# Performance work log

Hardware: AMD Instinct MI355X
Metric: run time of the kernel (lower is better)

The kernel has to match this reference:

```python
import jax, jax.numpy as jnp
import numpy as np

P, N, F, H, D_HID = 3, 4096, 1024, 8, 8
EMBED = H * D_HID  # 64
ATT, C = 128, 16


def setup_inputs() -> dict:
    key = jax.random.key(0)
    ks = jax.random.split(key, 12)
    return {
        "inputs": jax.random.normal(ks[0], (P, N, F), jnp.float32),
        # bias_mat plays the role of an additive adjacency mask; random floats are fine for math checking
        "bias_mat": jax.random.normal(ks[1], (P, N, N), jnp.float32),
        "W": jax.random.normal(ks[2], (P, H, F, D_HID), jnp.float32) * 0.05,
        "a1_w": jax.random.normal(ks[3], (P, H, D_HID), jnp.float32) * 0.1,
        "a1_b": jax.random.normal(ks[4], (P, H), jnp.float32) * 0.1,
        "a2_w": jax.random.normal(ks[5], (P, H, D_HID), jnp.float32) * 0.1,
        "a2_b": jax.random.normal(ks[6], (P, H), jnp.float32) * 0.1,
        "h_bias": jnp.zeros((P, H, D_HID), jnp.float32),
        "Ws": jax.random.normal(ks[7], (EMBED, ATT), jnp.float32) * 0.1,
        "bs": jax.random.normal(ks[8], (ATT,), jnp.float32) * 0.1,
        "u": jax.random.normal(ks[9], (ATT,), jnp.float32) * 0.1,
        "Wc": jax.random.normal(ks[10], (EMBED, C), jnp.float32) * 0.05,
        "bc": jnp.zeros((C,), jnp.float32),
    }


def reference(inputs, bias_mat, W, a1_w, a1_b, a2_w, a2_b, h_bias, Ws, bs, u, Wc, bc):
    # inputs: [P,N,F], bias_mat: [P,N,N]
    embeds = []
    for p in range(inputs.shape[0]):  # small fixed loop over meta-paths
        seq = inputs[p]                                            # [N,F]
        fts = jnp.einsum('nf,hfd->hnd', seq, W[p])                 # shared projection, all heads
        f1 = jnp.einsum('hnd,hd->hn', fts, a1_w[p]) + a1_b[p][:, None]
        f2 = jnp.einsum('hnd,hd->hn', fts, a2_w[p]) + a2_b[p][:, None]
        logits = f1[:, :, None] + f2[:, None, :]                   # [H,N,N] additive attention
        coefs = jax.nn.softmax(jax.nn.leaky_relu(logits) + bias_mat[p][None], axis=-1)
        vals = jnp.einsum('hnm,hmd->hnd', coefs, fts) + h_bias[p][:, None, :]
        h = jax.nn.elu(vals)                                       # activation per head
        embeds.append(jnp.transpose(h, (1, 0, 2)).reshape(h.shape[1], -1))  # concat heads -> [N,H*d]
    multi = jnp.stack(embeds, axis=1)                              # [N,P,EMBED]
    # semantic (meta-path) attention
    v = jnp.tanh(multi @ Ws + bs)                                  # [N,P,ATT]
    alphas = jax.nn.softmax(v @ u, axis=-1)                        # [N,P]
    final = jnp.sum(multi * alphas[:, :, None], axis=1)            # [N,EMBED]
    # single final classifier head (mean over 1 head == identity)
    logits_out = final @ Wc + bc                                   # [N,C]
    return logits_out, final, alphas
```

## Files before the change

kernel.cpp:

```cpp
#include <hip/hip_runtime.h>

#define LOG2E 1.44269504088896f

typedef _Float16 f16;
typedef _Float16 f16x8 __attribute__((ext_vector_type(8)));
typedef float f32x4 __attribute__((ext_vector_type(4)));

#define NP 3
#define NN 4096
#define FF 1024
#define HH 8
#define DD 8
#define HD 64

#define OFF_F1S   0
#define OFF_F2S   393216
#define OFF_F2MAX 589824
#define OFF_FTST  590080
#define OFF_MULTI 2162944

#define OUT_FINAL 65536
#define OUT_ALPHA 327680

__global__ __launch_bounds__(256) void kA(const float* __restrict__ inp,
                                          const float* __restrict__ W,
                                          const float* __restrict__ a1w,
                                          const float* __restrict__ a1b,
                                          const float* __restrict__ a2w,
                                          const float* __restrict__ a2b,
                                          char* __restrict__ ws) {
    __shared__ float At[32 * 34];
    __shared__ float Bt[32 * 64];
    __shared__ float ftile[32 * 68];
    const int tid = threadIdx.x;
    const int p = blockIdx.y;
    const int n0 = blockIdx.x * 32;

    const int tr = tid >> 4, tc = tid & 15;
    const int r0 = tr * 2, c0 = tc * 4;
    const int sr = tid >> 3, sak = (tid & 7) * 4;
    const int bk = tid >> 3, bh = tid & 7;

    const float* aP = inp + ((size_t)p * NN + n0 + sr) * FF + sak;
    const float* bP = W + (((size_t)p * HH + bh) * FF + bk) * DD;
    float* bDst = &Bt[bk * 64 + bh * 8];

    float4 pa, pb0, pb1;

#define KA_ISSUE(kb) do { \
        pa = *(const float4*)(aP + (kb) * 32); \
        const float* bp_ = bP + (size_t)(kb) * 32 * DD; \
        pb0 = *(const float4*)(bp_); \
        pb1 = *(const float4*)(bp_ + 4); \
    } while (0)

#define KA_COMMIT() do { \
        At[(sak + 0) * 34 + sr] = pa.x; \
        At[(sak + 1) * 34 + sr] = pa.y; \
        At[(sak + 2) * 34 + sr] = pa.z; \
        At[(sak + 3) * 34 + sr] = pa.w; \
        *(float4*)(bDst) = pb0; \
        *(float4*)(bDst + 4) = pb1; \
    } while (0)

    float acc[2][4] = {};

    KA_ISSUE(0);
    KA_COMMIT();
    KA_ISSUE(1);
    __syncthreads();

    #pragma unroll 1
    for (int kb = 0; kb < 32; ++kb) {
        #pragma unroll
        for (int k = 0; k < 32; ++k) {
            float2 a2 = *(const float2*)&At[k * 34 + r0];
            float4 bv = *(const float4*)&Bt[k * 64 + c0];
            float bb4[4] = {bv.x, bv.y, bv.z, bv.w};
            #pragma unroll
            for (int j = 0; j < 4; ++j) {
                acc[0][j] += a2.x * bb4[j];
                acc[1][j] += a2.y * bb4[j];
            }
        }
        __syncthreads();
        if (kb < 31) {
            KA_COMMIT();
            if (kb < 30) KA_ISSUE(kb + 2);
            __syncthreads();
        }
    }
#undef KA_ISSUE
#undef KA_COMMIT

    #pragma unroll
    for (int i = 0; i < 2; ++i) {
        float4 o;
        o.x = acc[i][0]; o.y = acc[i][1]; o.z = acc[i][2]; o.w = acc[i][3];
        *(float4*)&ftile[(r0 + i) * 68 + c0] = o;
    }
    __syncthreads();

    float* f1s = (float*)(ws + OFF_F1S);
    f16* f2s = (f16*)(ws + OFF_F2S);
    {
        int row = tid >> 3, h = tid & 7;
        const float* fb = &ftile[row * 68 + h * 8];
        float s1 = a1b[p * HH + h], s2 = a2b[p * HH + h];
        #pragma unroll
        for (int d = 0; d < 8; ++d) {
            float v = fb[d];
            s1 += v * a1w[((size_t)p * HH + h) * DD + d];
            s2 += v * a2w[((size_t)p * HH + h) * DD + d];
        }
        f1s[((size_t)p * HH + h) * NN + n0 + row] = s1 * LOG2E;
        f2s[((size_t)p * HH + h) * NN + n0 + row] = (f16)(s2 * LOG2E);
    }
    {
        f16* ftsT = (f16*)(ws + OFF_FTST);
        int cc2 = tid >> 2, rq = (tid & 3) * 8;
        union { f16 h[8]; uint4 u; } pk;
        #pragma unroll
        for (int i = 0; i < 8; ++i) pk.h[i] = (f16)ftile[(rq + i) * 68 + cc2];
        *(uint4*)(ftsT + ((size_t)p * HD + cc2) * NN + n0 + rq) = pk.u;
    }
}

__global__ __launch_bounds__(64) void kA2(char* __restrict__ ws) {
    const f16* f2s = (const f16*)(ws + OFF_F2S);
    float* fmax = (float*)(ws + OFF_F2MAX);
    int b = blockIdx.x;
    int lane = threadIdx.x;
    float v = -1e30f;
    for (int m = lane; m < NN; m += 64) v = fmaxf(v, (float)f2s[(size_t)b * NN + m]);
    #pragma unroll
    for (int off = 32; off >= 1; off >>= 1) v = fmaxf(v, __shfl_xor(v, off, 64));
    if (lane == 0) fmax[b] = v;
}

__global__ __launch_bounds__(256, 3) void kB(const float* __restrict__ bias,
                                             const float* __restrict__ h_bias,
                                             char* __restrict__ ws) {
    __shared__ __align__(16) char smem[42768];
    f16* ftsL = (f16*)smem;
    float* f2L = (float*)(smem + 34320);

    const int tid = threadIdx.x;
    const int lane = tid & 63, wv = tid >> 6;
    const int c = lane & 15, kg = lane >> 4;
    const int p = blockIdx.y;
    const int n0 = blockIdx.x * 16;
    const int n = n0 + c;

    const float* f1s = (const float*)(ws + OFF_F1S);
    const f16* f2s = (const f16*)(ws + OFF_F2S);
    const float* fmax = (const float*)(ws + OFF_F2MAX);
    const f16* ftsG = (const f16*)(ws + OFF_FTST);
    float* multi = (float*)(ws + OFF_MULTI);

    float A1[8], B1[8];
    #pragma unroll
    for (int h = 0; h < 8; ++h) {
        float f1v = f1s[((size_t)p * 8 + h) * NN + n];
        float fm = fmax[p * 8 + h];
        float x = f1v + fm;
        float lr = fmaxf(x, 0.01f * x);
        float ub = lr + 8.0f * LOG2E;
        A1[h] = f1v - ub;
        B1[h] = fmaf(0.01f, f1v, -ub);
    }

    for (int i = tid; i < 264; i += 256) ftsL[64 * 264 + i] = (f16)1.0f;

    const int sg = tid >> 3, se = tid & 7;
    const int srow = sg & 7, sq = sg >> 3;
    const int f2r = tid >> 5, f2c = (tid & 31) * 8;

    const f16* ftsP = ftsG + (size_t)p * HD * NN + sq * 64 + se * 8;
    const f16* f2P = f2s + (size_t)p * 8 * NN + (size_t)f2r * NN + f2c;
    f16* ldst = ftsL + srow * 264 + sq * 64 + se * 8;

    const int rowsel = (c < 8) ? c * 264 : 64 * 264;
    const int hstep = (c < 8) ? 8 * 264 : 0;

    const float* bb_base = bias + ((size_t)p * NN + n) * NN + wv * 64 + kg * 8;

    f32x4 acc[8] = {};

    uint4 r0, r1, r2, r3, r4, r5, r6, r7, rv;

#define ISSUE(ch) do { \
        const f16* gs_ = ftsP + (ch) * 256; \
        r0 = *(const uint4*)(gs_ + (size_t)(srow +  0) * NN); \
        r1 = *(const uint4*)(gs_ + (size_t)(srow +  8) * NN); \
        r2 = *(const uint4*)(gs_ + (size_t)(srow + 16) * NN); \
        r3 = *(const uint4*)(gs_ + (size_t)(srow + 24) * NN); \
        r4 = *(const uint4*)(gs_ + (size_t)(srow + 32) * NN); \
        r5 = *(const uint4*)(gs_ + (size_t)(srow + 40) * NN); \
        r6 = *(const uint4*)(gs_ + (size_t)(srow + 48) * NN); \
        r7 = *(const uint4*)(gs_ + (size_t)(srow + 56) * NN); \
        rv = *(const uint4*)(f2P + (ch) * 256); \
    } while (0)

#define COMMIT() do { \
        *(uint4*)(ldst + 0 * 8 * 264) = r0; \
        *(uint4*)(ldst + 1 * 8 * 264) = r1; \
        *(uint4*)(ldst + 2 * 8 * 264) = r2; \
        *(uint4*)(ldst + 3 * 8 * 264) = r3; \
        *(uint4*)(ldst + 4 * 8 * 264) = r4; \
        *(uint4*)(ldst + 5 * 8 * 264) = r5; \
        *(uint4*)(ldst + 6 * 8 * 264) = r6; \
        *(uint4*)(ldst + 7 * 8 * 264) = r7; \
        union { uint4 u; f16 h[8]; } t16_; \
        t16_.u = rv; \
        float4 lo_, hi_; \
        lo_.x = (float)t16_.h[0]; lo_.y = (float)t16_.h[1]; \
        lo_.z = (float)t16_.h[2]; lo_.w = (float)t16_.h[3]; \
        hi_.x = (float)t16_.h[4]; hi_.y = (float)t16_.h[5]; \
        hi_.z = (float)t16_.h[6]; hi_.w = (float)t16_.h[7]; \
        *(float4*)(f2L + f2r * 264 + f2c) = lo_; \
        *(float4*)(f2L + f2r * 264 + f2c + 4) = hi_; \
    } while (0)

    ISSUE(0);
    COMMIT();
    ISSUE(1);
    float4 uA0 = *(const float4*)(bb_base);
    float4 uA1 = *(const float4*)(bb_base + 4);
    float4 uB0 = *(const float4*)(bb_base + 32);
    float4 uB1 = *(const float4*)(bb_base + 36);
    __syncthreads();

    #pragma unroll 1
    for (int ch = 0; ch < 16; ++ch) {
        const int chn = (ch + 1 < 16) ? ch + 1 : 15;
        const float* bpn = bb_base + chn * 256;
        float4 nA0 = *(const float4*)(bpn);
        float4 nA1 = *(const float4*)(bpn + 4);
        float4 nB0 = *(const float4*)(bpn + 32);
        float4 nB1 = *(const float4*)(bpn + 36);

        #pragma unroll
        for (int s = 0; s < 2; ++s) {
            const int mloc = wv * 64 + s * 32 + kg * 8;
            float4 bv0 = s ? uB0 : uA0;
            float4 bv1 = s ? uB1 : uA1;
            float bbl[8] = {bv0.x * LOG2E, bv0.y * LOG2E, bv0.z * LOG2E, bv0.w * LOG2E,
                            bv1.x * LOG2E, bv1.y * LOG2E, bv1.z * LOG2E, bv1.w * LOG2E};
            #pragma unroll
            for (int h = 0; h < 8; ++h) {
                const float* f2p = f2L + h * 264 + mloc;
                float4 f2a = *(const float4*)f2p;
                float4 f2b = *(const float4*)(f2p + 4);
                float f2arr[8] = {f2a.x, f2a.y, f2a.z, f2a.w, f2b.x, f2b.y, f2b.z, f2b.w};
                f16x8 bf = *(const f16x8*)(ftsL + rowsel + h * hstep + mloc);
                union { f16x8 v; f16 e[8]; } af;
                #pragma unroll
                for (int j = 0; j < 8; ++j) {
                    float t1 = f2arr[j] + A1[h];
                    float t2 = fmaf(0.01f, f2arr[j], B1[h]);
                    af.e[j] = (f16)__builtin_amdgcn_exp2f(fmaxf(t1, t2) + bbl[j]);
                }
                acc[h] = __builtin_amdgcn_mfma_f32_16x16x32_f16(af.v, bf, acc[h], 0, 0, 0);
            }
        }
        __syncthreads();
        if (ch < 15) {
            COMMIT();
            if (ch < 14) ISSUE(ch + 2);
            __syncthreads();
        }
        uA0 = nA0; uA1 = nA1; uB0 = nB0; uB1 = nB1;
    }
#undef ISSUE
#undef COMMIT

    float* red = (float*)smem;
    #pragma unroll
    for (int h = 0; h < 8; ++h) {
        if (c <= 8) {
            #pragma unroll
            for (int r = 0; r < 4; ++r)
                red[((wv * 8 + h) * 16 + kg * 4 + r) * 9 + c] = acc[h][r];
        }
    }
    __syncthreads();
    #pragma unroll
    for (int rep = 0; rep < 4; ++rep) {
        int idx = tid + rep * 256;
        int R = idx >> 6, hd = idx & 63;
        int h = hd >> 3, d = hd & 7;
        float v = 0.f, l = 0.f;
        #pragma unroll
        for (int w = 0; w < 4; ++w) {
            v += red[((w * 8 + h) * 16 + R) * 9 + d];
            l += red[((w * 8 + h) * 16 + R) * 9 + 8];
        }
        float o = v / l + h_bias[(p * 8 + h) * 8 + d];
        o = o > 0.f ? o : (__builtin_amdgcn_exp2f(o * LOG2E) - 1.0f);
        multi[((size_t)(n0 + R) * NP + p) * HD + hd] = o;
    }
}

__global__ __launch_bounds__(256) void kC(const float* __restrict__ Ws,
                                          const float* __restrict__ bsv,
                                          const float* __restrict__ uv,
                                          const float* __restrict__ Wc,
                                          const float* __restrict__ bcv,
                                          char* __restrict__ ws,
                                          float* __restrict__ out) {
    __shared__ float WsL[64 * 128];
    __shared__ float mult[16 * 3 * 64];
    __shared__ float WcL[64 * 16];
    __shared__ float uL[128], bsL[128], bcL[16];
    __shared__ float vred[16 * 3 * 16];
    __shared__ float alphaL[16 * 3];
    __shared__ float fin[16 * 64];
    const int tid = threadIdx.x;
    const int n0 = blockIdx.x * 16;
    const float* multi = (const float*)(ws + OFF_MULTI);

    for (int i = tid; i < 64 * 128; i += 256) WsL[i] = Ws[i];
    for (int i = tid; i < 3072; i += 256) mult[i] = multi[(size_t)n0 * 192 + i];
    for (int i = tid; i < 1024; i += 256) WcL[i] = Wc[i];
    if (tid < 128) { uL[tid] = uv[tid]; bsL[tid] = bsv[tid]; }
    if (tid < 16) bcL[tid] = bcv[tid];
    __syncthreads();

    const int nl = tid >> 4, j = tid & 15;
    for (int p = 0; p < 3; ++p) {
        float va[8] = {};
        for (int e = 0; e < 64; ++e) {
            float me = mult[(nl * 3 + p) * 64 + e];
            #pragma unroll
            for (int i = 0; i < 8; ++i) va[i] += me * WsL[e * 128 + j + 16 * i];
        }
        float part = 0.f;
        #pragma unroll
        for (int i = 0; i < 8; ++i) part += tanhf(va[i] + bsL[j + 16 * i]) * uL[j + 16 * i];
        vred[(nl * 3 + p) * 16 + j] = part;
    }
    __syncthreads();
    if (tid < 16) {
        float sc[3];
        for (int p = 0; p < 3; ++p) {
            float s = 0.f;
            for (int jj = 0; jj < 16; ++jj) s += vred[(tid * 3 + p) * 16 + jj];
            sc[p] = s;
        }
        float mx = fmaxf(sc[0], fmaxf(sc[1], sc[2]));
        float e0 = __builtin_amdgcn_exp2f((sc[0] - mx) * LOG2E);
        float e1 = __builtin_amdgcn_exp2f((sc[1] - mx) * LOG2E);
        float e2 = __builtin_amdgcn_exp2f((sc[2] - mx) * LOG2E);
        float inv = 1.f / (e0 + e1 + e2);
        float a0 = e0 * inv, a1 = e1 * inv, a2 = e2 * inv;
        alphaL[tid * 3 + 0] = a0; alphaL[tid * 3 + 1] = a1; alphaL[tid * 3 + 2] = a2;
        out[OUT_ALPHA + (size_t)(n0 + tid) * 3 + 0] = a0;
        out[OUT_ALPHA + (size_t)(n0 + tid) * 3 + 1] = a1;
        out[OUT_ALPHA + (size_t)(n0 + tid) * 3 + 2] = a2;
    }
    __syncthreads();
    for (int idx = tid; idx < 1024; idx += 256) {
        int nn2 = idx >> 6, e = idx & 63;
        float f = 0.f;
        for (int p = 0; p < 3; ++p) f += mult[(nn2 * 3 + p) * 64 + e] * alphaL[nn2 * 3 + p];
        fin[nn2 * 64 + e] = f;
        out[OUT_FINAL + (size_t)(n0 + nn2) * 64 + e] = f;
    }
    __syncthreads();
    {
        int nn2 = tid >> 4, cc2 = tid & 15;
        float lg = bcL[cc2];
        for (int e = 0; e < 64; ++e) lg += fin[nn2 * 64 + e] * WcL[e * 16 + cc2];
        out[(size_t)(n0 + nn2) * 16 + cc2] = lg;
    }
}

extern "C" void kernel_launch(void* const* d_in, const int* in_sizes, int n_in,
                              void* d_out, int out_size, void* d_ws, size_t ws_size,
                              hipStream_t stream) {
    (void)in_sizes; (void)n_in; (void)out_size; (void)ws_size;
    const float* inp = (const float*)d_in[0];
    const float* bias = (const float*)d_in[1];
    const float* W = (const float*)d_in[2];
    const float* a1w = (const float*)d_in[3];
    const float* a1b = (const float*)d_in[4];
    const float* a2w = (const float*)d_in[5];
    const float* a2b = (const float*)d_in[6];
    const float* hb = (const float*)d_in[7];
    const float* Wsv = (const float*)d_in[8];
    const float* bsv = (const float*)d_in[9];
    const float* uv = (const float*)d_in[10];
    const float* Wcv = (const float*)d_in[11];
    const float* bcv = (const float*)d_in[12];
    char* ws = (char*)d_ws;
    float* out = (float*)d_out;

    hipLaunchKernelGGL(kA, dim3(128, 3), dim3(256), 0, stream, inp, W, a1w, a1b, a2w, a2b, ws);
    hipLaunchKernelGGL(kA2, dim3(24), dim3(64), 0, stream, ws);
    hipLaunchKernelGGL(kB, dim3(256, 3), dim3(256), 0, stream, bias, hb, ws);
    hipLaunchKernelGGL(kC, dim3(256), dim3(256), 0, stream, Wsv, bsv, uv, Wcv, bcv, ws, out);
}
```

Measured before the change: 413.7 us.

## Split projection GEMM along K into two slabs with separate reduction epilogue kernel

The projection GEMM kernel is split along the F dimension into two halves (grid z=2), each writing partial fp32 results to workspace slabs. A new epilogue kernel sums the slabs and computes f1/f2 and the transposed fp16 features. This doubles the block count so the GPU is better filled (384 blocks before), at the cost of an extra launch and slab write/read traffic. The f2 max kernel also switches to vectorized 16-byte loads.

```diff
diff --git a/kernel.cpp b/kernel.cpp
--- a/kernel.cpp
+++ b/kernel.cpp
@@ -18,23 +18,22 @@
 #define OFF_F2MAX 589824
 #define OFF_FTST  590080
 #define OFF_MULTI 2162944
+#define OFF_FP0   2162944
+#define OFF_FP1   5308672
+#define SLAB_BYTES 3145728
 
 #define OUT_FINAL 65536
 #define OUT_ALPHA 327680
 
-__global__ __launch_bounds__(256) void kA(const float* __restrict__ inp,
-                                          const float* __restrict__ W,
-                                          const float* __restrict__ a1w,
-                                          const float* __restrict__ a1b,
-                                          const float* __restrict__ a2w,
-                                          const float* __restrict__ a2b,
-                                          char* __restrict__ ws) {
+__global__ __launch_bounds__(256) void kA1(const float* __restrict__ inp,
+                                           const float* __restrict__ W,
+                                           char* __restrict__ ws) {
     __shared__ float At[32 * 34];
     __shared__ float Bt[32 * 64];
-    __shared__ float ftile[32 * 68];
     const int tid = threadIdx.x;
     const int p = blockIdx.y;
     const int n0 = blockIdx.x * 32;
+    const int kb0 = blockIdx.z * 16;
 
     const int tr = tid >> 4, tc = tid & 15;
     const int r0 = tr * 2, c0 = tc * 4;
@@ -44,6 +43,7 @@
     const float* aP = inp + ((size_t)p * NN + n0 + sr) * FF + sak;
     const float* bP = W + (((size_t)p * HH + bh) * FF + bk) * DD;
     float* bDst = &Bt[bk * 64 + bh * 8];
+    float* slab = (float*)(ws + OFF_FP0 + (size_t)blockIdx.z * SLAB_BYTES);
 
     float4 pa, pb0, pb1;
 
@@ -65,13 +65,13 @@
 
     float acc[2][4] = {};
 
-    KA_ISSUE(0);
+    KA_ISSUE(kb0);
     KA_COMMIT();
-    KA_ISSUE(1);
+    KA_ISSUE(kb0 + 1);
     __syncthreads();
 
     #pragma unroll 1
-    for (int kb = 0; kb < 32; ++kb) {
+    for (int kb = 0; kb < 16; ++kb) {
         #pragma unroll
         for (int k = 0; k < 32; ++k) {
             float2 a2 = *(const float2*)&At[k * 34 + r0];
@@ -84,9 +84,9 @@
             }
         }
         __syncthreads();
-        if (kb < 31) {
+        if (kb < 15) {
             KA_COMMIT();
-            if (kb < 30) KA_ISSUE(kb + 2);
+            if (kb < 14) KA_ISSUE(kb0 + kb + 2);
             __syncthreads();
         }
     }
@@ -97,32 +97,63 @@
     for (int i = 0; i < 2; ++i) {
         float4 o;
         o.x = acc[i][0]; o.y = acc[i][1]; o.z = acc[i][2]; o.w = acc[i][3];
-        *(float4*)&ftile[(r0 + i) * 68 + c0] = o;
+        *(float4*)(slab + ((size_t)p * NN + n0 + r0 + i) * HD + c0) = o;
+    }
+}
+
+__global__ __launch_bounds__(256) void kAe(const float* __restrict__ a1w,
+                                           const float* __restrict__ a1b,
+                                           const float* __restrict__ a2w,
+                                           const float* __restrict__ a2b,
+                                           char* __restrict__ ws) {
+    __shared__ float ftile[64 * 68];
+    const int tid = threadIdx.x;
+    const int p = blockIdx.y;
+    const int n0 = blockIdx.x * 64;
+
+    const float* s0 = (const float*)(ws + OFF_FP0) + ((size_t)p * NN + n0) * HD;
+    const float* s1 = (const float*)(ws + OFF_FP1) + ((size_t)p * NN + n0) * HD;
+
+    {
+        const int base = tid * 16;
+        const int row = base >> 6, col = base & 63;
+        #pragma unroll
+        for (int q = 0; q < 4; ++q) {
+            float4 u = *(const float4*)(s0 + base + q * 4);
+            float4 v = *(const float4*)(s1 + base + q * 4);
+            float4 o;
+            o.x = u.x + v.x; o.y = u.y + v.y; o.z = u.z + v.z; o.w = u.w + v.w;
+            *(float4*)&ftile[row * 68 + col + q * 4] = o;
+        }
     }
     __syncthreads();
 
     float* f1s = (float*)(ws + OFF_F1S);
     f16* f2s = (f16*)(ws + OFF_F2S);
-    {
-        int row = tid >> 3, h = tid & 7;
+    #pragma unroll
+    for (int rep = 0; rep < 2; ++rep) {
+        int task = tid + rep * 256;
+        int row = task >> 3, h = task & 7;
         const float* fb = &ftile[row * 68 + h * 8];
-        float s1 = a1b[p * HH + h], s2 = a2b[p * HH + h];
+        float s1v = a1b[p * HH + h], s2v = a2b[p * HH + h];
         #pragma unroll
         for (int d = 0; d < 8; ++d) {
             float v = fb[d];
-            s1 += v * a1w[((size_t)p * HH + h) * DD + d];
-            s2 += v * a2w[((size_t)p * HH + h) * DD + d];
-        }
-        f1s[((size_t)p * HH + h) * NN + n0 + row] = s1 * LOG2E;
-        f2s[((size_t)p * HH + h) * NN + n0 + row] = (f16)(s2 * LOG2E);
+            s1v += v * a1w[((size_t)p * HH + h) * DD + d];
+            s2v += v * a2w[((size_t)p * HH + h) * DD + d];
+        }
+        f1s[((size_t)p * HH + h) * NN + n0 + row] = s1v * LOG2E;
+        f2s[((size_t)p * HH + h) * NN + n0 + row] = (f16)(s2v * LOG2E);
     }
     {
         f16* ftsT = (f16*)(ws + OFF_FTST);
-        int cc2 = tid >> 2, rq = (tid & 3) * 8;
-        union { f16 h[8]; uint4 u; } pk;
-        #pragma unroll
-        for (int i = 0; i < 8; ++i) pk.h[i] = (f16)ftile[(rq + i) * 68 + cc2];
-        *(uint4*)(ftsT + ((size_t)p * HD + cc2) * NN + n0 + rq) = pk.u;
+        int cc2 = tid >> 2, rq = (tid & 3) * 16;
+        union { f16 h[16]; uint4 u[2]; } pk;
+        #pragma unroll
+        for (int i = 0; i < 16; ++i) pk.h[i] = (f16)ftile[(rq + i) * 68 + cc2];
+        uint4* dst = (uint4*)(ftsT + ((size_t)p * HD + cc2) * NN + n0 + rq);
+        dst[0] = pk.u[0];
+        dst[1] = pk.u[1];
     }
 }
 
@@ -132,7 +163,13 @@
     int b = blockIdx.x;
     int lane = threadIdx.x;
     float v = -1e30f;
-    for (int m = lane; m < NN; m += 64) v = fmaxf(v, (float)f2s[(size_t)b * NN + m]);
+    #pragma unroll
+    for (int it = 0; it < 8; ++it) {
+        union { uint4 u; f16 h[8]; } t;
+        t.u = *(const uint4*)(f2s + (size_t)b * NN + ((size_t)it * 64 + lane) * 8);
+        #pragma unroll
+        for (int j = 0; j < 8; ++j) v = fmaxf(v, (float)t.h[j]);
+    }
     #pragma unroll
     for (int off = 32; off >= 1; off >>= 1) v = fmaxf(v, __shfl_xor(v, off, 64));
     if (lane == 0) fmax[b] = v;
@@ -396,7 +433,8 @@
     char* ws = (char*)d_ws;
     float* out = (float*)d_out;
 
-    hipLaunchKernelGGL(kA, dim3(128, 3), dim3(256), 0, stream, inp, W, a1w, a1b, a2w, a2b, ws);
+    hipLaunchKernelGGL(kA1, dim3(128, 3, 2), dim3(256), 0, stream, inp, W, ws);
+    hipLaunchKernelGGL(kAe, dim3(64, 3), dim3(256), 0, stream, a1w, a1b, a2w, a2b, ws);
     hipLaunchKernelGGL(kA2, dim3(24), dim3(64), 0, stream, ws);
     hipLaunchKernelGGL(kB, dim3(256, 3), dim3(256), 0, stream, bias, hb, ws);
     hipLaunchKernelGGL(kC, dim3(256), dim3(256), 0, stream, Wsv, bsv, uv, Wcv, bcv, ws, out);
```

Measured after the change: 399.2 us. 3.5% less time.
